# Kernel tuning notes

Hardware: AMD Instinct MI355X
Metric: run time of the kernel (lower is better)

Reference implementation:

```python
import jax, jax.numpy as jnp
import numpy as np

BOUND = 10.0
EPS = 1e-06
MIN_SCALE = 1e-4


def _params_to_spline(raw_w, raw_h, raw_s, bound):
    # Standard Durkan et al. rational-quadratic spline parameterization.
    # raw_w/raw_h: (1, D, K); raw_s: (1, D, K+1)
    two_b = 2.0 * bound
    widths = jax.nn.softmax(raw_w[0], axis=-1) * two_b      # (D, K)
    heights = jax.nn.softmax(raw_h[0], axis=-1) * two_b     # (D, K)
    zero = jnp.zeros(widths.shape[:-1] + (1,), widths.dtype)
    xk = -bound + jnp.concatenate([zero, jnp.cumsum(widths, axis=-1)], axis=-1)   # (D, K+1)
    yk = -bound + jnp.concatenate([zero, jnp.cumsum(heights, axis=-1)], axis=-1)  # (D, K+1)
    slopes = jax.nn.softplus(raw_s[0])                       # (D, K+1)
    return xk, yk, widths, heights, slopes


def _rqs_forward(z, xk, yk, widths, heights, slopes, bound):
    # z: (B, D); per-dim knots xk/yk: (D, K+1); widths/heights: (D, K); slopes: (D, K+1)
    B, D = z.shape
    K = widths.shape[-1]
    zc = jnp.clip(z, -bound, bound)
    # per-dim binary search over knot positions
    idx = jax.vmap(lambda knots, col: jnp.searchsorted(knots, col, side='right'),
                   in_axes=(0, 1), out_axes=1)(xk, zc) - 1
    idx = jnp.clip(idx, 0, K - 1)                            # (B, D)
    di = jnp.arange(D)[None, :]
    xk_sel = xk[di, idx]
    w_sel = widths[di, idx]
    yk_sel = yk[di, idx]
    h_sel = heights[di, idx]
    d0 = slopes[di, idx]
    d1 = slopes[di, idx + 1]
    theta = (zc - xk_sel) / w_sel
    s = h_sel / w_sel
    t1m = theta * (1.0 - theta)
    den = s + (d0 + d1 - 2.0 * s) * t1m
    y_in = yk_sel + h_sel * (s * theta * theta + d0 * t1m) / den
    inside = (z > -bound) & (z < bound)
    return jnp.where(inside, y_in, z)


def setup_inputs() -> dict:
    key = jax.random.key(0)
    ks = jax.random.split(key, 7)
    B, D, K = 8192, 1024, 64
    return {
        'u': jax.random.uniform(ks[0], (B, D), dtype=jnp.float32),
        'tau': jax.random.normal(ks[1], (B, 1), dtype=jnp.float32),
        'log_scale': jax.random.normal(ks[2], (D,), dtype=jnp.float32) * 0.1,
        'bias': jax.random.normal(ks[3], (D,), dtype=jnp.float32) * 0.1,
        'raw_w': jax.random.normal(ks[4], (1, D, K), dtype=jnp.float32) * 0.5,
        'raw_h': jax.random.normal(ks[5], (1, D, K), dtype=jnp.float32) * 0.5,
        'raw_s': jax.random.normal(ks[6], (1, D, K + 1), dtype=jnp.float32) * 0.5,
    }


def reference(u, tau, log_scale, bias, raw_w, raw_h, raw_s):
    # logit input transform
    u_safe = jnp.clip(u, EPS, 1.0 - EPS)
    z = jnp.log(u_safe) - jnp.log1p(-u_safe)
    xk, yk, widths, heights, slopes = _params_to_spline(raw_w, raw_h, raw_s, BOUND)
    z = _rqs_forward(z, xk, yk, widths, heights, slopes, BOUND)
    scale = jax.nn.softplus(log_scale) + MIN_SCALE
    q = z * scale[None, :] + bias[None, :]
    return tau * q  # tau (B,1) broadcasts to (B,D)
```

## Files before the change

kernel.cpp:

```cpp
#include <hip/hip_runtime.h>
#include <math.h>

#define BOUNDF 10.0f
#define EPSF 1e-6f
#define MIN_SCALEF 1e-4f
#define DD 1024
#define KK 64
#define KP1 65

#define TD 32
#define TR 128

__global__ __launch_bounds__(64) void rqs_precompute(
    const float* __restrict__ raw_w, const float* __restrict__ raw_h,
    const float* __restrict__ raw_s, const float* __restrict__ log_scale,
    float* __restrict__ xk, float* __restrict__ yk,
    float* __restrict__ sl, float* __restrict__ scale)
{
    const int d = blockIdx.x;
    const int k = threadIdx.x;

    float ew = __expf(raw_w[d * KK + k]);
    float eh = __expf(raw_h[d * KK + k]);

    float sw = ew, sh = eh;
#pragma unroll
    for (int off = 1; off < 64; off <<= 1) {
        sw += __shfl_xor(sw, off, 64);
        sh += __shfl_xor(sh, off, 64);
    }
    float wk = ew * (2.0f * BOUNDF) / sw;
    float hk = eh * (2.0f * BOUNDF) / sh;

    float cw = wk, ch = hk;
#pragma unroll
    for (int off = 1; off < 64; off <<= 1) {
        float tw = __shfl_up(cw, off, 64);
        float th = __shfl_up(ch, off, 64);
        if (k >= off) { cw += tw; ch += th; }
    }
    xk[d * KP1 + k + 1] = -BOUNDF + cw;
    yk[d * KP1 + k + 1] = -BOUNDF + ch;

    float rs = raw_s[d * KP1 + k];
    sl[d * KP1 + k] = log1pf(__expf(rs));
    if (k == 0) {
        xk[d * KP1] = -BOUNDF;
        yk[d * KP1] = -BOUNDF;
        float rs2 = raw_s[d * KP1 + KK];
        sl[d * KP1 + KK] = log1pf(__expf(rs2));
        scale[d] = log1pf(__expf(log_scale[d])) + MIN_SCALEF;
    }
}

__global__ __launch_bounds__(256, 6) void rqs_main(
    const float* __restrict__ u, const float* __restrict__ tau,
    const float* __restrict__ bias,
    const float* __restrict__ xk_g, const float* __restrict__ yk_g,
    const float* __restrict__ sl_g, const float* __restrict__ scale_g,
    float* __restrict__ out)
{
    __shared__ float lxk[TD * KP1];
    __shared__ float lyk[TD * KP1];
    __shared__ float lsl[TD * KP1];

    const int bx = blockIdx.x;
    const int dchunk = bx & (DD / TD - 1);
    const int rchunk = bx >> 5;
    const int d0 = dchunk * TD;
    const int r0 = rchunk * TR;
    const int t = threadIdx.x;

    for (int i = t; i < TD * KP1; i += 256) {
        lxk[i] = xk_g[d0 * KP1 + i];
        lyk[i] = yk_g[d0 * KP1 + i];
        lsl[i] = sl_g[d0 * KP1 + i];
    }
    __syncthreads();

    const int g = t & 7;
    const int rlane = t >> 3;
    const int dl = g * 4;
    const int dg = d0 + dl;

    float sc[4], bi[4];
    float kreg[4][7];
#pragma unroll
    for (int j = 0; j < 4; ++j) {
        sc[j] = scale_g[dg + j];
        bi[j] = bias[dg + j];
        const int base = (dl + j) * KP1;
#pragma unroll
        for (int i = 0; i < 7; ++i) kreg[j][i] = lxk[base + 8 * (i + 1)];
    }

    int b = r0 + rlane;
    float4 uu = *(const float4*)(u + (size_t)b * DD + dg);
    float tb = tau[b];

#pragma unroll 1
    for (int it = 0; it < TR / 32; ++it) {
        const int bcur = b;
        const float4 ucur = uu;
        const float tcur = tb;
        if (it + 1 < TR / 32) {
            const int bn = bcur + 32;
            uu = *(const float4*)(u + (size_t)bn * DD + dg);
            tb = tau[bn];
            b = bn;
        }
        float ua[4] = {ucur.x, ucur.y, ucur.z, ucur.w};
        float res[4];
#pragma unroll
        for (int j = 0; j < 4; ++j) {
            float uv = fminf(fmaxf(ua[j], EPSF), 1.0f - EPSF);
            float z = __logf(uv * __builtin_amdgcn_rcpf(1.0f - uv));
            float zc = fminf(fmaxf(z, -BOUNDF), BOUNDF);
            const int base = (dl + j) * KP1;
            int lo = (zc >= kreg[j][3]) ? 32 : 0;
            float m16 = (lo & 32) ? kreg[j][5] : kreg[j][1];
            lo += (zc >= m16) ? 16 : 0;
            float a8 = (lo & 32) ? kreg[j][4] : kreg[j][0];
            float b8 = (lo & 32) ? kreg[j][6] : kreg[j][2];
            float m8 = (lo & 16) ? b8 : a8;
            lo += (zc >= m8) ? 8 : 0;
            lo += (lxk[base + lo + 4] <= zc) ? 4 : 0;
            lo += (lxk[base + lo + 2] <= zc) ? 2 : 0;
            lo += (lxk[base + lo + 1] <= zc) ? 1 : 0;
            float x0 = lxk[base + lo], x1 = lxk[base + lo + 1];
            float y0 = lyk[base + lo], y1 = lyk[base + lo + 1];
            float s0 = lsl[base + lo], s1 = lsl[base + lo + 1];
            float w = x1 - x0, h = y1 - y0;
            float invw = __builtin_amdgcn_rcpf(w);
            float th = (zc - x0) * invw;
            float sm = h * invw;
            float t1m = th * (1.0f - th);
            float den = fmaf(fmaf(-2.0f, sm, s0 + s1), t1m, sm);
            float num = h * fmaf(sm * th, th, s0 * t1m);
            float y = fmaf(num, __builtin_amdgcn_rcpf(den), y0);
            y = (z > -BOUNDF && z < BOUNDF) ? y : z;
            res[j] = tcur * fmaf(y, sc[j], bi[j]);
        }
        float4 ro = make_float4(res[0], res[1], res[2], res[3]);
        *(float4*)(out + (size_t)bcur * DD + dg) = ro;
    }
}

extern "C" void kernel_launch(void* const* d_in, const int* in_sizes, int n_in,
                              void* d_out, int out_size, void* d_ws, size_t ws_size,
                              hipStream_t stream)
{
    const float* u         = (const float*)d_in[0];
    const float* tau       = (const float*)d_in[1];
    const float* log_scale = (const float*)d_in[2];
    const float* bias      = (const float*)d_in[3];
    const float* raw_w     = (const float*)d_in[4];
    const float* raw_h     = (const float*)d_in[5];
    const float* raw_s     = (const float*)d_in[6];
    float* out = (float*)d_out;

    float* ws    = (float*)d_ws;
    float* xk    = ws;
    float* yk    = xk + DD * KP1;
    float* sl    = yk + DD * KP1;
    float* scale = sl + DD * KP1;

    const int B = in_sizes[0] / DD;

    rqs_precompute<<<DD, 64, 0, stream>>>(raw_w, raw_h, raw_s, log_scale,
                                          xk, yk, sl, scale);
    rqs_main<<<(DD / TD) * (B / TR), 256, 0, stream>>>(u, tau, bias,
                                                       xk, yk, sl, scale, out);
}
```

Before: 111.0 us.

## Shrink tiles to 16 dims x 64 rows, use float2 nontemporal IO and full unroll

Halves the dimension tile to 16 and the row tile to 64, so each thread handles 2 dims via float2 instead of 4 via float4, which raises the block count and LDS-limited occupancy (launch bound raised to 8). The LDS spline tables are staged with vector loads, the manual software prefetch is replaced by a fully unrolled row loop, and u loads and out stores become nontemporal. This shortens per-block LDS setup and improves latency hiding, in exchange for narrower global accesses and more blocks each reloading spline tables.

After: 121.1 us. 1.09x slower.

```diff
diff --git a/kernel.cpp b/kernel.cpp
--- a/kernel.cpp
+++ b/kernel.cpp
@@ -8,8 +8,10 @@
 #define KK 64
 #define KP1 65
 
-#define TD 32
-#define TR 128
+#define TD 16
+#define TR 64
+
+typedef float vf2 __attribute__((ext_vector_type(2)));
 
 __global__ __launch_bounds__(64) void rqs_precompute(
     const float* __restrict__ raw_w, const float* __restrict__ raw_h,
@@ -53,7 +55,7 @@
     }
 }
 
-__global__ __launch_bounds__(256, 6) void rqs_main(
+__global__ __launch_bounds__(256, 8) void rqs_main(
     const float* __restrict__ u, const float* __restrict__ tau,
     const float* __restrict__ bias,
     const float* __restrict__ xk_g, const float* __restrict__ yk_g,
@@ -66,27 +68,35 @@
 
     const int bx = blockIdx.x;
     const int dchunk = bx & (DD / TD - 1);
-    const int rchunk = bx >> 5;
+    const int rchunk = bx >> 6;
     const int d0 = dchunk * TD;
     const int r0 = rchunk * TR;
     const int t = threadIdx.x;
 
-    for (int i = t; i < TD * KP1; i += 256) {
-        lxk[i] = xk_g[d0 * KP1 + i];
-        lyk[i] = yk_g[d0 * KP1 + i];
-        lsl[i] = sl_g[d0 * KP1 + i];
+    {
+        const vf2* sx = (const vf2*)(xk_g + d0 * KP1);
+        const vf2* sy = (const vf2*)(yk_g + d0 * KP1);
+        const vf2* ss = (const vf2*)(sl_g + d0 * KP1);
+        vf2* dx = (vf2*)lxk;
+        vf2* dy = (vf2*)lyk;
+        vf2* dsl = (vf2*)lsl;
+        for (int i = t; i < TD * KP1 / 2; i += 256) {
+            dx[i] = sx[i];
+            dy[i] = sy[i];
+            dsl[i] = ss[i];
+        }
     }
     __syncthreads();
 
     const int g = t & 7;
     const int rlane = t >> 3;
-    const int dl = g * 4;
+    const int dl = g * 2;
     const int dg = d0 + dl;
 
-    float sc[4], bi[4];
-    float kreg[4][7];
+    float sc[2], bi[2];
+    float kreg[2][7];
 #pragma unroll
-    for (int j = 0; j < 4; ++j) {
+    for (int j = 0; j < 2; ++j) {
         sc[j] = scale_g[dg + j];
         bi[j] = bias[dg + j];
         const int base = (dl + j) * KP1;
@@ -94,25 +104,16 @@
         for (int i = 0; i < 7; ++i) kreg[j][i] = lxk[base + 8 * (i + 1)];
     }
 
-    int b = r0 + rlane;
-    float4 uu = *(const float4*)(u + (size_t)b * DD + dg);
-    float tb = tau[b];
-
-#pragma unroll 1
+#pragma unroll
     for (int it = 0; it < TR / 32; ++it) {
-        const int bcur = b;
-        const float4 ucur = uu;
-        const float tcur = tb;
-        if (it + 1 < TR / 32) {
-            const int bn = bcur + 32;
-            uu = *(const float4*)(u + (size_t)bn * DD + dg);
-            tb = tau[bn];
-            b = bn;
-        }
-        float ua[4] = {ucur.x, ucur.y, ucur.z, ucur.w};
-        float res[4];
+        const int b = r0 + it * 32 + rlane;
+        const vf2 uu = __builtin_nontemporal_load(
+            (const vf2*)(u + (size_t)b * DD + dg));
+        const float tb = tau[b];
+        float ua[2] = {uu.x, uu.y};
+        float res[2];
 #pragma unroll
-        for (int j = 0; j < 4; ++j) {
+        for (int j = 0; j < 2; ++j) {
             float uv = fminf(fmaxf(ua[j], EPSF), 1.0f - EPSF);
             float z = __logf(uv * __builtin_amdgcn_rcpf(1.0f - uv));
             float zc = fminf(fmaxf(z, -BOUNDF), BOUNDF);
@@ -139,10 +140,12 @@
             float num = h * fmaf(sm * th, th, s0 * t1m);
             float y = fmaf(num, __builtin_amdgcn_rcpf(den), y0);
             y = (z > -BOUNDF && z < BOUNDF) ? y : z;
-            res[j] = tcur * fmaf(y, sc[j], bi[j]);
+            res[j] = tb * fmaf(y, sc[j], bi[j]);
         }
-        float4 ro = make_float4(res[0], res[1], res[2], res[3]);
-        *(float4*)(out + (size_t)bcur * DD + dg) = ro;
+        vf2 ro;
+        ro.x = res[0];
+        ro.y = res[1];
+        __builtin_nontemporal_store(ro, (vf2*)(out + (size_t)b * DD + dg));
     }
 }
 
```
